# Optimization experiments

Hardware: AMD Instinct MI355X
Metric: run time of the kernel (lower is better)

The kernel has to match this reference:

```python
import math
import jax, jax.numpy as jnp
import numpy as np

N = 4096        # stocks in cross-section
T = 64          # lookback window
D_FEAT = 158
D_MARKET = 64
D_EMB = 32
D_MODEL = 256
T_NHEAD = 4
S_NHEAD = 4
BETA = 1.0
MAX_LEN = 100


def _pe_table(max_len, d_model):
    pos = np.arange(max_len, dtype=np.float32)[:, None]
    div = np.exp(np.arange(0, d_model, 2, dtype=np.float32) * (-math.log(10000.0) / d_model))
    pe = np.zeros((max_len, d_model), dtype=np.float32)
    pe[:, 0::2] = np.sin(pos * div)
    pe[:, 1::2] = np.cos(pos * div)
    return jnp.asarray(pe)


def setup_inputs() -> dict:
    key = jax.random.key(0)
    ks = jax.random.split(key, 24)
    w = lambda k, shape: jax.random.normal(k, shape, jnp.float32) * 0.02
    inp = {
        'industry_ids': jax.random.randint(ks[0], (N,), 0, 256),
        'stock_features': jax.random.normal(ks[1], (N, T, D_FEAT), jnp.float32),
        'market_features': jax.random.normal(ks[2], (N, T, D_MARKET), jnp.float32),
        'gate_W': w(ks[3], (D_MARKET, D_FEAT)), 'gate_b': jnp.zeros((D_FEAT,), jnp.float32),
        'emb_table': w(ks[4], (256, D_EMB)),
        'proj_W': w(ks[5], (D_FEAT, D_MODEL)), 'proj_b': jnp.zeros((D_MODEL,), jnp.float32),
        'pe': _pe_table(MAX_LEN, D_MODEL),
        'ta_qW': w(ks[6], (D_MODEL, D_MODEL)), 'ta_kW': w(ks[7], (D_MODEL, D_MODEL)), 'ta_vW': w(ks[8], (D_MODEL, D_MODEL)),
        'ta_n1_g': jnp.ones((D_MODEL,), jnp.float32), 'ta_n1_b': jnp.zeros((D_MODEL,), jnp.float32),
        'ta_n2_g': jnp.ones((D_MODEL,), jnp.float32), 'ta_n2_b': jnp.zeros((D_MODEL,), jnp.float32),
        'ta_f1W': w(ks[9], (D_MODEL, D_MODEL)), 'ta_f1b': jnp.zeros((D_MODEL,), jnp.float32),
        'ta_f2W': w(ks[10], (D_MODEL, D_MODEL)), 'ta_f2b': jnp.zeros((D_MODEL,), jnp.float32),
        'agg_W': w(ks[11], (D_MODEL, D_MODEL)),
        'sa_qW': w(ks[12], (D_MODEL + D_EMB, D_MODEL)), 'sa_kW': w(ks[13], (D_MODEL + D_EMB, D_MODEL)),
        'sa_vW': w(ks[14], (D_MODEL, D_MODEL)),
        'sa_n1_g': jnp.ones((D_MODEL,), jnp.float32), 'sa_n1_b': jnp.zeros((D_MODEL,), jnp.float32),
        'sa_n2_g': jnp.ones((D_EMB,), jnp.float32), 'sa_n2_b': jnp.zeros((D_EMB,), jnp.float32),
        'sa_n3_g': jnp.ones((D_MODEL,), jnp.float32), 'sa_n3_b': jnp.zeros((D_MODEL,), jnp.float32),
        'sa_f1W': w(ks[15], (D_MODEL, D_MODEL)), 'sa_f1b': jnp.zeros((D_MODEL,), jnp.float32),
        'sa_f2W': w(ks[16], (D_MODEL, D_MODEL)), 'sa_f2b': jnp.zeros((D_MODEL,), jnp.float32),
        'dec_W': w(ks[17], (D_MODEL, 1)), 'dec_b': jnp.zeros((1,), jnp.float32),
    }
    return inp


def _ln(x, g, b, eps=1e-5):
    m = x.mean(-1, keepdims=True)
    v = ((x - m) ** 2).mean(-1, keepdims=True)
    return (x - m) * jax.lax.rsqrt(v + eps) * g + b


def reference(industry_ids, stock_features, market_features, gate_W, gate_b,
              emb_table, proj_W, proj_b, pe,
              ta_qW, ta_kW, ta_vW, ta_n1_g, ta_n1_b, ta_n2_g, ta_n2_b,
              ta_f1W, ta_f1b, ta_f2W, ta_f2b,
              agg_W,
              sa_qW, sa_kW, sa_vW, sa_n1_g, sa_n1_b, sa_n2_g, sa_n2_b,
              sa_n3_g, sa_n3_b, sa_f1W, sa_f1b, sa_f2W, sa_f2b,
              dec_W, dec_b):
    n, t = stock_features.shape[0], stock_features.shape[1]
    # ---- market gating + embedding + projection + positional encoding ----
    emb = emb_table[industry_ids]                                   # [N, d_emb]
    mkt = market_features[:, -1, :]                                 # [N, d_market]
    gate = D_FEAT * jax.nn.softmax((mkt @ gate_W + gate_b) / BETA, axis=-1)
    x = stock_features * gate[:, None, :]                           # [N, T, d_feat]
    x = x @ proj_W + proj_b + pe[:t]                                # [N, T, d_model]
    # ---- TAttention (per-head temporal attention, no temperature scale) ----
    xn = _ln(x, ta_n1_g, ta_n1_b)
    hd = D_MODEL // T_NHEAD
    q = (xn @ ta_qW).reshape(n, t, T_NHEAD, hd)
    k = (xn @ ta_kW).reshape(n, t, T_NHEAD, hd)
    v = (xn @ ta_vW).reshape(n, t, T_NHEAD, hd)
    attn = jax.nn.softmax(jnp.einsum('nthd,nshd->nhts', q, k), axis=-1)
    ao = jnp.einsum('nhts,nshd->nthd', attn, v).reshape(n, t, D_MODEL)
    xt = xn + ao
    ffn = jax.nn.relu(_ln(xt, ta_n2_g, ta_n2_b) @ ta_f1W + ta_f1b) @ ta_f2W + ta_f2b
    x = xt + ffn                                                    # [N, T, d_model]
    # ---- TemporalAttention aggregation ----
    h = x @ agg_W                                                   # [N, T, d_model]
    lam = jax.nn.softmax(jnp.einsum('ntd,nd->nt', h, h[:, -1, :]), axis=1)
    z = jnp.einsum('nt,ntd->nd', lam, x)                            # [N, d_model]
    # ---- SAttention (cross-sectional attention over stocks) ----
    zn = _ln(z, sa_n1_g, sa_n1_b)
    en = _ln(emb, sa_n2_g, sa_n2_b)
    qk_in = jnp.concatenate([zn, en], axis=-1)                      # [N, d_model+d_emb]
    shd = D_MODEL // S_NHEAD
    q2 = (qk_in @ sa_qW).reshape(n, S_NHEAD, shd)
    k2 = (qk_in @ sa_kW).reshape(n, S_NHEAD, shd)
    v2 = (zn @ sa_vW).reshape(n, S_NHEAD, shd)
    scores = jnp.einsum('nhd,mhd->hnm', q2, k2) / math.sqrt(shd)    # [H, N, N]
    a2 = jax.nn.softmax(scores, axis=-1)
    o2 = jnp.einsum('hnm,mhd->nhd', a2, v2).reshape(n, D_MODEL)
    xt2 = zn + o2
    ffn2 = jax.nn.relu(_ln(xt2, sa_n3_g, sa_n3_b) @ sa_f1W + sa_f1b) @ sa_f2W + sa_f2b
    out = xt2 + ffn2
    # ---- decoder ----
    return out @ dec_W + dec_b                                      # [N, 1]
```

## Files before the change

### kernel.cpp

```cpp
#include <hip/hip_runtime.h>
#include <math.h>

typedef unsigned int uint32;
typedef unsigned short ushort;

typedef __bf16 bf16x8 __attribute__((ext_vector_type(8)));
typedef float f32x4 __attribute__((ext_vector_type(4)));

#define DEV static __device__ __forceinline__

DEV float bf2f(ushort u){ return __builtin_bit_cast(float, ((uint32)u) << 16); }
DEV ushort f2bf(float f){
  uint32 i = __builtin_bit_cast(uint32, f);
  uint32 r = i + 0x7fffu + ((i >> 16) & 1u);
  return (ushort)(r >> 16);
}
DEV float wsum(float v){
  #pragma unroll
  for (int off = 32; off > 0; off >>= 1) v += __shfl_xor(v, off);
  return v;
}

__global__ void k_detect(const ushort* pe, const ushort* n1g, int* dt){
  if (threadIdx.x==0 && blockIdx.x==0){
    int isb = (pe[1]==0x3F80u && n1g[0]==0x3F80u) ? 1 : 0;
    *dt = isb ? 1 : 0;
  }
}

struct CvtArgs { const void* src[33]; ushort* dst[33]; int n[33]; };
__global__ __launch_bounds__(256) void k_cvtbatch(CvtArgs a, const int* dtp){
  int z = blockIdx.y;
  int i = blockIdx.x*256 + threadIdx.x;
  if (i >= a.n[z]) return;
  int sdt = *dtp;
  a.dst[z][i] = sdt ? ((const ushort*)a.src[z])[i] : f2bf(((const float*)a.src[z])[i]);
}

struct TrArgs { const ushort* src[12]; ushort* dst[12]; int ldsrc[12]; int R[12]; int C[12]; int lddst[12]; int RP[12]; };
__global__ __launch_bounds__(256) void k_trbatch(TrArgs a){
  int z = blockIdx.z;
  __shared__ ushort tile[32][33];
  int tx = threadIdx.x & 31, ty = threadIdx.x >> 5;
  int rb = blockIdx.x * 32, cb = blockIdx.y * 32;
  const ushort* src = a.src[z];
  int ld_src = a.ldsrc[z], R = a.R[z], C = a.C[z];
  #pragma unroll
  for (int i = 0; i < 4; i++){
    int r = rb + ty + i*8, c = cb + tx;
    ushort v = 0;
    if (r < R && c < C) v = src[(size_t)r*ld_src + c];
    tile[ty + i*8][tx] = v;
  }
  __syncthreads();
  ushort* dst = a.dst[z];
  int ld_dst = a.lddst[z], RP = a.RP[z];
  #pragma unroll
  for (int i = 0; i < 4; i++){
    int c = cb + ty + i*8, r = rb + tx;
    if (c < C && r < RP) dst[(size_t)c*ld_dst + r] = tile[tx][ty + i*8];
  }
}

__global__ __launch_bounds__(256) void k_transpose(const ushort* __restrict__ src, int ld_src,
    int R, int C, ushort* __restrict__ dst, int ld_dst, int RP)
{
  __shared__ ushort tile[32][33];
  int tx = threadIdx.x & 31, ty = threadIdx.x >> 5;
  int rb = blockIdx.x * 32, cb = blockIdx.y * 32;
  #pragma unroll
  for (int i = 0; i < 4; i++){
    int r = rb + ty + i*8, c = cb + tx;
    ushort v = 0;
    if (r < R && c < C) v = src[(size_t)r*ld_src + c];
    tile[ty + i*8][tx] = v;
  }
  __syncthreads();
  #pragma unroll
  for (int i = 0; i < 4; i++){
    int c = cb + ty + i*8, r = rb + tx;
    if (c < C && r < RP) dst[(size_t)c*ld_dst + r] = tile[tx][ty + i*8];
  }
}

__global__ __launch_bounds__(256) void k_gate(const void* __restrict__ mfv,
    const ushort* __restrict__ gW, const ushort* __restrict__ gb, float* __restrict__ gate,
    const int* dtp)
{
  int n = blockIdx.x, tid = threadIdx.x;
  __shared__ int sdt;
  __shared__ float mkt[64];
  __shared__ float red[256];
  if (tid == 0) sdt = *dtp;
  __syncthreads();
  if (tid < 64){
    size_t idx = ((size_t)n*64 + 63)*64 + tid;
    mkt[tid] = sdt ? bf2f(((const ushort*)mfv)[idx]) : ((const float*)mfv)[idx];
  }
  __syncthreads();
  float lg = -1e30f;
  if (tid < 158){
    float a = bf2f(gb[tid]);
    #pragma unroll 8
    for (int d = 0; d < 64; d++) a += mkt[d] * bf2f(gW[d*158 + tid]);
    lg = a;
  }
  red[tid] = lg; __syncthreads();
  for (int s = 128; s > 0; s >>= 1){ if (tid < s) red[tid] = fmaxf(red[tid], red[tid+s]); __syncthreads(); }
  float mx = red[0]; __syncthreads();
  float p = (tid < 158) ? __expf(lg - mx) : 0.f;
  red[tid] = p; __syncthreads();
  for (int s = 128; s > 0; s >>= 1){ if (tid < s) red[tid] += red[tid+s]; __syncthreads(); }
  float inv = 158.f / red[0];
  if (tid < 158) gate[(size_t)n*158 + tid] = p * inv;
}

__global__ __launch_bounds__(256) void k_ag(const void* __restrict__ sfv, size_t rowoff,
    const float* __restrict__ gate_c, ushort* __restrict__ Ag, int total, const int* dtp)
{
  __shared__ int sdt;
  if (threadIdx.x == 0) sdt = *dtp;
  __syncthreads();
  int idx = blockIdx.x*256 + threadIdx.x;
  if (idx >= total) return;
  int row = idx / 160;
  int d = idx - row*160;
  float v = 0.f;
  if (d < 158){
    int n = row >> 6;
    size_t si = (rowoff + (size_t)row)*158 + d;
    float s = sdt ? bf2f(((const ushort*)sfv)[si]) : ((const float*)sfv)[si];
    v = s * gate_c[(size_t)n*158 + d];
  }
  Ag[idx] = f2bf(v);
}

template<int BM, int BN>
__global__ __launch_bounds__(256) void k_gemm(
    const ushort* __restrict__ A, int lda,
    const ushort* __restrict__ WT, int ldw,
    ushort* __restrict__ C, int ldc,
    const ushort* __restrict__ bias,
    const ushort* __restrict__ resid, int ldr,
    const ushort* __restrict__ pe,
    float scale, int relu, int K)
{
  __shared__ ushort As[BM*40];
  __shared__ ushort Bs[BN*40];

  const int tid = threadIdx.x;
  const int wave = tid >> 6, lane = tid & 63;
  const int quad = lane >> 4, l16 = lane & 15;
  constexpr int WC = BN/64;
  const int wr = wave / WC, wc = wave % WC;
  const int m0 = blockIdx.x * BM, n0 = blockIdx.y * BN;

  f32x4 acc[4][4];
  #pragma unroll
  for (int i = 0; i < 4; i++)
    #pragma unroll
    for (int j = 0; j < 4; j++)
      acc[i][j] = f32x4{0.f, 0.f, 0.f, 0.f};

  for (int k0 = 0; k0 < K; k0 += 32){
    __syncthreads();
    #pragma unroll
    for (int i = 0; i < BM/64; i++){
      int ch = tid + i*256;
      int r = ch >> 2, cw = (ch & 3)*8;
      *reinterpret_cast<uint4*>(&As[r*40 + cw]) =
        *reinterpret_cast<const uint4*>(A + (size_t)(m0+r)*lda + k0 + cw);
    }
    #pragma unroll
    for (int i = 0; i < BN/64; i++){
      int ch = tid + i*256;
      int r = ch >> 2, cw = (ch & 3)*8;
      *reinterpret_cast<uint4*>(&Bs[r*40 + cw]) =
        *reinterpret_cast<const uint4*>(WT + (size_t)(n0+r)*ldw + k0 + cw);
    }
    __syncthreads();
    bf16x8 af[4], bfr[4];
    #pragma unroll
    for (int t = 0; t < 4; t++){
      af[t]  = *reinterpret_cast<const bf16x8*>(&As[(wr*64 + t*16 + l16)*40 + quad*8]);
      bfr[t] = *reinterpret_cast<const bf16x8*>(&Bs[(wc*64 + t*16 + l16)*40 + quad*8]);
    }
    #pragma unroll
    for (int mt = 0; mt < 4; mt++)
      #pragma unroll
      for (int nt = 0; nt < 4; nt++)
        acc[mt][nt] = __builtin_amdgcn_mfma_f32_16x16x32_bf16(af[mt], bfr[nt], acc[mt][nt], 0, 0, 0);
  }

  #pragma unroll
  for (int mt = 0; mt < 4; mt++){
    #pragma unroll
    for (int nt = 0; nt < 4; nt++){
      int col = n0 + wc*64 + nt*16 + l16;
      #pragma unroll
      for (int r = 0; r < 4; r++){
        int row = m0 + wr*64 + mt*16 + quad*4 + r;
        float v = acc[mt][nt][r] * scale;
        if (bias)  v += bf2f(bias[col]);
        if (pe)    v += bf2f(pe[(row & 63)*256 + col]);
        if (relu)  v = fmaxf(v, 0.f);
        if (resid) v += bf2f(resid[(size_t)row*ldr + col]);
        C[(size_t)row*ldc + col] = f2bf(v);
      }
    }
  }
}

__global__ __launch_bounds__(256) void k_ln(const ushort* __restrict__ x,
    const ushort* __restrict__ g, const ushort* __restrict__ b, ushort* __restrict__ y)
{
  int row = blockIdx.x*4 + (threadIdx.x >> 6);
  int lane = threadIdx.x & 63;
  ushort4 u = *reinterpret_cast<const ushort4*>(x + (size_t)row*256 + lane*4);
  float v0 = bf2f(u.x), v1 = bf2f(u.y), v2 = bf2f(u.z), v3 = bf2f(u.w);
  float s = wsum(v0+v1+v2+v3);
  float q = wsum(v0*v0+v1*v1+v2*v2+v3*v3);
  float mean = s * (1.f/256.f);
  float var  = fmaxf(q * (1.f/256.f) - mean*mean, 0.f);
  float rs = rsqrtf(var + 1e-5f);
  ushort4 gg = *reinterpret_cast<const ushort4*>(g + lane*4);
  ushort4 bb = *reinterpret_cast<const ushort4*>(b + lane*4);
  ushort4 o;
  o.x = f2bf((v0-mean)*rs*bf2f(gg.x) + bf2f(bb.x));
  o.y = f2bf((v1-mean)*rs*bf2f(gg.y) + bf2f(bb.y));
  o.z = f2bf((v2-mean)*rs*bf2f(gg.z) + bf2f(bb.z));
  o.w = f2bf((v3-mean)*rs*bf2f(gg.w) + bf2f(bb.w));
  *reinterpret_cast<ushort4*>(y + (size_t)row*256 + lane*4) = o;
}

__global__ __launch_bounds__(64) void k_tattn(
    const ushort* __restrict__ q, const ushort* __restrict__ k,
    const ushort* __restrict__ v, ushort* __restrict__ xnxt)
{
  int n = blockIdx.x >> 2, h = blockIdx.x & 3;
  int lane = threadIdx.x;
  int quad = lane >> 4, l16 = lane & 15;
  __shared__ ushort Pl[64*72];
  __shared__ ushort Vt[64*72];
  size_t base = ((size_t)n*64)*256 + (size_t)h*64;

  f32x4 accs[4][4];
  #pragma unroll
  for (int i = 0; i < 4; i++)
    #pragma unroll
    for (int j = 0; j < 4; j++)
      accs[i][j] = f32x4{0.f, 0.f, 0.f, 0.f};

  #pragma unroll
  for (int ks = 0; ks < 64; ks += 32){
    bf16x8 qf[4], kf[4];
    #pragma unroll
    for (int tt = 0; tt < 4; tt++){
      qf[tt] = *reinterpret_cast<const bf16x8*>(q + base + (size_t)(tt*16 + l16)*256 + ks + quad*8);
      kf[tt] = *reinterpret_cast<const bf16x8*>(k + base + (size_t)(tt*16 + l16)*256 + ks + quad*8);
    }
    #pragma unroll
    for (int mt = 0; mt < 4; mt++)
      #pragma unroll
      for (int nt = 0; nt < 4; nt++)
        accs[mt][nt] = __builtin_amdgcn_mfma_f32_16x16x32_bf16(qf[mt], kf[nt], accs[mt][nt], 0, 0, 0);
  }

  for (int s = 0; s < 64; s++)
    Vt[lane*72 + s] = v[base + (size_t)s*256 + lane];

  #pragma unroll
  for (int mt = 0; mt < 4; mt++){
    #pragma unroll
    for (int r = 0; r < 4; r++){
      float a0 = accs[mt][0][r], a1 = accs[mt][1][r], a2 = accs[mt][2][r], a3 = accs[mt][3][r];
      float mx = fmaxf(fmaxf(a0, a1), fmaxf(a2, a3));
      #pragma unroll
      for (int off = 1; off < 16; off <<= 1) mx = fmaxf(mx, __shfl_xor(mx, off));
      float e0 = __expf(a0-mx), e1 = __expf(a1-mx), e2 = __expf(a2-mx), e3 = __expf(a3-mx);
      float sum = e0+e1+e2+e3;
      #pragma unroll
      for (int off = 1; off < 16; off <<= 1) sum += __shfl_xor(sum, off);
      float inv = 1.f/sum;
      int t = mt*16 + quad*4 + r;
      Pl[t*72 +  0 + l16] = f2bf(e0*inv);
      Pl[t*72 + 16 + l16] = f2bf(e1*inv);
      Pl[t*72 + 32 + l16] = f2bf(e2*inv);
      Pl[t*72 + 48 + l16] = f2bf(e3*inv);
    }
  }
  __syncthreads();

  f32x4 acco[4][4];
  #pragma unroll
  for (int i = 0; i < 4; i++)
    #pragma unroll
    for (int j = 0; j < 4; j++)
      acco[i][j] = f32x4{0.f, 0.f, 0.f, 0.f};

  #pragma unroll
  for (int ks = 0; ks < 64; ks += 32){
    bf16x8 pf[4], vf[4];
    #pragma unroll
    for (int tt = 0; tt < 4; tt++){
      pf[tt] = *reinterpret_cast<const bf16x8*>(&Pl[(tt*16 + l16)*72 + ks + quad*8]);
      vf[tt] = *reinterpret_cast<const bf16x8*>(&Vt[(tt*16 + l16)*72 + ks + quad*8]);
    }
    #pragma unroll
    for (int mt = 0; mt < 4; mt++)
      #pragma unroll
      for (int nt = 0; nt < 4; nt++)
        acco[mt][nt] = __builtin_amdgcn_mfma_f32_16x16x32_bf16(pf[mt], vf[nt], acco[mt][nt], 0, 0, 0);
  }

  #pragma unroll
  for (int mt = 0; mt < 4; mt++)
    #pragma unroll
    for (int nt = 0; nt < 4; nt++)
      #pragma unroll
      for (int r = 0; r < 4; r++){
        int t = mt*16 + quad*4 + r, d = nt*16 + l16;
        size_t g = base + (size_t)t*256 + d;
        xnxt[g] = f2bf(bf2f(xnxt[g]) + acco[mt][nt][r]);
      }
}

__global__ __launch_bounds__(256) void k_lamz(const ushort* __restrict__ h,
    const ushort* __restrict__ x2, float* __restrict__ z)
{
  int n = blockIdx.x, tid = threadIdx.x, wave = tid >> 6, lane = tid & 63;
  __shared__ float hl[256];
  __shared__ float dotv[64];
  __shared__ float lamv[64];
  hl[tid] = bf2f(h[((size_t)n*64 + 63)*256 + tid]);
  __syncthreads();
  float h0 = hl[lane*4], h1 = hl[lane*4+1], h2 = hl[lane*4+2], h3 = hl[lane*4+3];
  for (int tt = 0; tt < 16; tt++){
    int t = wave*16 + tt;
    ushort4 u = *reinterpret_cast<const ushort4*>(h + ((size_t)n*64 + t)*256 + lane*4);
    float p = bf2f(u.x)*h0 + bf2f(u.y)*h1 + bf2f(u.z)*h2 + bf2f(u.w)*h3;
    p = wsum(p);
    if (lane == 0) dotv[t] = p;
  }
  __syncthreads();
  if (wave == 0){
    float vv = dotv[lane];
    float mx = vv;
    #pragma unroll
    for (int off = 32; off > 0; off >>= 1) mx = fmaxf(mx, __shfl_xor(mx, off));
    float e = __expf(vv - mx);
    float s = wsum(e);
    lamv[lane] = e / s;
  }
  __syncthreads();
  float acc = 0.f;
  for (int t = 0; t < 64; t++) acc += lamv[t] * bf2f(x2[((size_t)n*64 + t)*256 + tid]);
  z[(size_t)n*256 + tid] = acc;
}

__global__ __launch_bounds__(64) void k_prep(const float* __restrict__ z,
    const int* __restrict__ ids, const ushort* __restrict__ emb,
    const ushort* __restrict__ g1, const ushort* __restrict__ b1,
    const ushort* __restrict__ g2, const ushort* __restrict__ b2,
    ushort* __restrict__ zn, ushort* __restrict__ qkin)
{
  int n = blockIdx.x, lane = threadIdx.x;
  float4 v = *reinterpret_cast<const float4*>(z + (size_t)n*256 + lane*4);
  float s = wsum(v.x+v.y+v.z+v.w);
  float q = wsum(v.x*v.x+v.y*v.y+v.z*v.z+v.w*v.w);
  float mean = s*(1.f/256.f);
  float var = fmaxf(q*(1.f/256.f) - mean*mean, 0.f);
  float rs = rsqrtf(var + 1e-5f);
  ushort4 gg = *reinterpret_cast<const ushort4*>(g1 + lane*4);
  ushort4 bb = *reinterpret_cast<const ushort4*>(b1 + lane*4);
  ushort4 o;
  o.x = f2bf((v.x-mean)*rs*bf2f(gg.x) + bf2f(bb.x));
  o.y = f2bf((v.y-mean)*rs*bf2f(gg.y) + bf2f(bb.y));
  o.z = f2bf((v.z-mean)*rs*bf2f(gg.z) + bf2f(bb.z));
  o.w = f2bf((v.w-mean)*rs*bf2f(gg.w) + bf2f(bb.w));
  *reinterpret_cast<ushort4*>(zn + (size_t)n*256 + lane*4) = o;
  *reinterpret_cast<ushort4*>(qkin + (size_t)n*288 + lane*4) = o;
  int id = ids[n];
  float ev = (lane < 32) ? bf2f(emb[(size_t)id*32 + lane]) : 0.f;
  float se = ev, sq = ev*ev;
  #pragma unroll
  for (int off = 1; off < 32; off <<= 1){ se += __shfl_xor(se, off); sq += __shfl_xor(sq, off); }
  if (lane < 32){
    float m2 = se*(1.f/32.f);
    float va = fmaxf(sq*(1.f/32.f) - m2*m2, 0.f);
    float r2 = rsqrtf(va + 1e-5f);
    qkin[(size_t)n*288 + 256 + lane] = f2bf((ev-m2)*r2*bf2f(g2[lane]) + bf2f(b2[lane]));
  }
}

__global__ __launch_bounds__(256) void k_xattn(
    const ushort* __restrict__ qk, const ushort* __restrict__ vT,
    const ushort* __restrict__ zn, ushort* __restrict__ xt2)
{
  int rb = blockIdx.x, h = blockIdx.y;
  int tid = threadIdx.x, wave = tid >> 6, lane = tid & 63;
  int quad = lane >> 4, l16 = lane & 15;
  int q0 = rb*64 + wave*16;

  bf16x8 qf[2];
  #pragma unroll
  for (int s = 0; s < 2; s++)
    qf[s] = *reinterpret_cast<const bf16x8*>(qk + (size_t)(q0 + l16)*512 + h*64 + s*32 + quad*8);

  float m[4]  = {-1e30f,-1e30f,-1e30f,-1e30f};
  float l[4]  = {0.f,0.f,0.f,0.f};
  f32x4 acc[4];
  #pragma unroll
  for (int nd = 0; nd < 4; nd++) acc[nd] = f32x4{0.f,0.f,0.f,0.f};

  __shared__ ushort Pl[4][16*72];

  for (int kt = 0; kt < 64; kt++){
    int kb = kt*64;
    f32x4 s4[4];
    #pragma unroll
    for (int nt = 0; nt < 4; nt++){
      f32x4 a = f32x4{0.f,0.f,0.f,0.f};
      #pragma unroll
      for (int s = 0; s < 2; s++){
        bf16x8 kf = *reinterpret_cast<const bf16x8*>(
            qk + (size_t)(kb + nt*16 + l16)*512 + 256 + h*64 + s*32 + quad*8);
        a = __builtin_amdgcn_mfma_f32_16x16x32_bf16(qf[s], kf, a, 0, 0, 0);
      }
      s4[nt] = a;
    }
    float alpha[4];
    #pragma unroll
    for (int r = 0; r < 4; r++){
      float v0 = s4[0][r]*0.125f, v1 = s4[1][r]*0.125f, v2 = s4[2][r]*0.125f, v3 = s4[3][r]*0.125f;
      float mx = fmaxf(fmaxf(v0,v1), fmaxf(v2,v3));
      #pragma unroll
      for (int off = 1; off < 16; off <<= 1) mx = fmaxf(mx, __shfl_xor(mx, off));
      float mnew = fmaxf(m[r], mx);
      alpha[r] = __expf(m[r] - mnew);
      float e0 = __expf(v0-mnew), e1 = __expf(v1-mnew), e2 = __expf(v2-mnew), e3 = __expf(v3-mnew);
      float ps = e0+e1+e2+e3;
      #pragma unroll
      for (int off = 1; off < 16; off <<= 1) ps += __shfl_xor(ps, off);
      l[r] = l[r]*alpha[r] + ps;
      m[r] = mnew;
      int t = quad*4 + r;
      Pl[wave][t*72 +  0 + l16] = f2bf(e0);
      Pl[wave][t*72 + 16 + l16] = f2bf(e1);
      Pl[wave][t*72 + 32 + l16] = f2bf(e2);
      Pl[wave][t*72 + 48 + l16] = f2bf(e3);
    }
    #pragma unroll
    for (int nd = 0; nd < 4; nd++)
      #pragma unroll
      for (int r = 0; r < 4; r++)
        acc[nd][r] *= alpha[r];
    __syncthreads();
    #pragma unroll
    for (int s = 0; s < 2; s++){
      bf16x8 pf = *reinterpret_cast<const bf16x8*>(&Pl[wave][l16*72 + s*32 + quad*8]);
      #pragma unroll
      for (int nd = 0; nd < 4; nd++){
        bf16x8 vf = *reinterpret_cast<const bf16x8*>(
            vT + (size_t)(h*64 + nd*16 + l16)*4096 + kb + s*32 + quad*8);
        acc[nd] = __builtin_amdgcn_mfma_f32_16x16x32_bf16(pf, vf, acc[nd], 0, 0, 0);
      }
    }
    __syncthreads();
  }

  #pragma unroll
  for (int nd = 0; nd < 4; nd++)
    #pragma unroll
    for (int r = 0; r < 4; r++){
      int row = q0 + quad*4 + r;
      int col = h*64 + nd*16 + l16;
      float val = acc[nd][r] / l[r] + bf2f(zn[(size_t)row*256 + col]);
      xt2[(size_t)row*256 + col] = f2bf(val);
    }
}

__global__ __launch_bounds__(64) void k_decode(const ushort* __restrict__ xv,
    const ushort* __restrict__ dW, const ushort* __restrict__ db, void* out, const int* dtp)
{
  int n = blockIdx.x, lane = threadIdx.x;
  ushort4 u = *reinterpret_cast<const ushort4*>(xv + (size_t)n*256 + lane*4);
  ushort4 w = *reinterpret_cast<const ushort4*>(dW + lane*4);
  float acc = bf2f(u.x)*bf2f(w.x) + bf2f(u.y)*bf2f(w.y) + bf2f(u.z)*bf2f(w.z) + bf2f(u.w)*bf2f(w.w);
  acc = wsum(acc);
  if (lane == 0){
    float r = acc + bf2f(db[0]);
    if (*dtp) ((ushort*)out)[n] = f2bf(r);
    else      ((float*)out)[n]  = r;
  }
}

extern "C" void kernel_launch(void* const* d_in, const int* in_sizes, int n_in,
                              void* d_out, int out_size, void* d_ws, size_t ws_size,
                              hipStream_t stream)
{
  (void)in_sizes; (void)n_in; (void)out_size;
  const int*  ids = (const int*)d_in[0];
  const void* sf  = d_in[1];
  const void* mf  = d_in[2];

  auto padsz = [](size_t b)->size_t{ return (b + 255) & ~(size_t)255; };
  size_t fixedB = padsz((size_t)4096*158*4) + padsz((size_t)4096*256*4)
                + 6*padsz((size_t)4096*256*2)
                + padsz((size_t)4096*512*2)
                + padsz((size_t)256*4096*2)
                + padsz((size_t)4096*288*2)
                + (size_t)4*1024*1024;
  auto tierB = [&](int NCp)->size_t{
    size_t MCp = (size_t)NCp*64;
    return fixedB + 4*padsz(MCp*256*2) + padsz(MCp*160*2);
  };
  int NC = 64;
  if      (tierB(4096) <= ws_size) NC = 4096;
  else if (tierB(1024) <= ws_size) NC = 1024;
  else if (tierB(256)  <= ws_size) NC = 256;
  const int NCHUNK = 4096 / NC;
  const int MC = NC * 64;

  char* ws = (char*)d_ws;
  size_t off = 0;
  auto alloc = [&](size_t bytes)->char*{ char* p = ws + off; off += (bytes + 255) & ~(size_t)255; return p; };
  int* dt = (int*)alloc(256);
  ushort* C0 = (ushort*)alloc((size_t)MC*256*2);
  ushort* C1 = (ushort*)alloc((size_t)MC*256*2);
  ushort* C2 = (ushort*)alloc((size_t)MC*256*2);
  ushort* C3 = (ushort*)alloc((size_t)MC*256*2);
  ushort* Ag = (ushort*)alloc((size_t)MC*160*2);
  float*  gate = (float*)alloc((size_t)4096*158*4);
  float*  z    = (float*)alloc((size_t)4096*256*4);
  ushort* zn   = (ushort*)alloc((size_t)4096*256*2);
  ushort* q2k2 = (ushort*)alloc((size_t)4096*512*2);
  ushort* v2   = (ushort*)alloc((size_t)4096*256*2);
  ushort* vT   = (ushort*)alloc((size_t)256*4096*2);
  ushort* xt2  = (ushort*)alloc((size_t)4096*256*2);
  ushort* n3   = (ushort*)alloc((size_t)4096*256*2);
  ushort* h2   = (ushort*)alloc((size_t)4096*256*2);
  ushort* xv   = (ushort*)alloc((size_t)4096*256*2);
  ushort* qkin = (ushort*)alloc((size_t)4096*288*2);

  auto cvalloc = [&](int n)->ushort*{ return (ushort*)alloc((size_t)n*2); };
  ushort* gWc   = cvalloc(64*158);
  ushort* gbc   = cvalloc(158);
  ushort* embc  = cvalloc(256*32);
  ushort* projWc= cvalloc(158*256);
  ushort* projbc= cvalloc(256);
  ushort* pec   = cvalloc(100*256);
  ushort* taqWc = cvalloc(65536);
  ushort* takWc = cvalloc(65536);
  ushort* tavWc = cvalloc(65536);
  ushort* n1gc  = cvalloc(256);
  ushort* n1bc  = cvalloc(256);
  ushort* n2gc  = cvalloc(256);
  ushort* n2bc  = cvalloc(256);
  ushort* f1Wc  = cvalloc(65536);
  ushort* f1bc  = cvalloc(256);
  ushort* f2Wc  = cvalloc(65536);
  ushort* f2bc  = cvalloc(256);
  ushort* aggWc = cvalloc(65536);
  ushort* saqWc = cvalloc(288*256);
  ushort* sakWc = cvalloc(288*256);
  ushort* savWc = cvalloc(65536);
  ushort* sn1gc = cvalloc(256);
  ushort* sn1bc = cvalloc(256);
  ushort* sn2gc = cvalloc(32);
  ushort* sn2bc = cvalloc(32);
  ushort* sn3gc = cvalloc(256);
  ushort* sn3bc = cvalloc(256);
  ushort* sf1Wc = cvalloc(65536);
  ushort* sf1bc = cvalloc(256);
  ushort* sf2Wc = cvalloc(65536);
  ushort* sf2bc = cvalloc(256);
  ushort* decWc = cvalloc(256);
  ushort* decbc = cvalloc(1);
  ushort* projWT = cvalloc(256*160);
  ushort* taqWT  = cvalloc(65536);
  ushort* takWT  = cvalloc(65536);
  ushort* tavWT  = cvalloc(65536);
  ushort* f1WT   = cvalloc(65536);
  ushort* f2WT   = cvalloc(65536);
  ushort* aggWT  = cvalloc(65536);
  ushort* savWT  = cvalloc(65536);
  ushort* sf1WT  = cvalloc(65536);
  ushort* sf2WT  = cvalloc(65536);
  ushort* qk2WT  = cvalloc(512*288);

  dim3 b256(256), b64(64);

  k_detect<<<1, 64, 0, stream>>>((const ushort*)d_in[8], (const ushort*)d_in[12], dt);

  CvtArgs ca;
  int ci = 0;
  auto addcv = [&](int idx, ushort* dst, int n){ ca.src[ci]=d_in[idx]; ca.dst[ci]=dst; ca.n[ci]=n; ci++; };
  addcv(3,  gWc,   64*158);  addcv(4,  gbc,   158);     addcv(5,  embc,  256*32);
  addcv(6,  projWc,158*256); addcv(7,  projbc,256);     addcv(8,  pec,   100*256);
  addcv(9,  taqWc, 65536);   addcv(10, takWc, 65536);   addcv(11, tavWc, 65536);
  addcv(12, n1gc,  256);     addcv(13, n1bc,  256);     addcv(14, n2gc,  256);
  addcv(15, n2bc,  256);     addcv(16, f1Wc,  65536);   addcv(17, f1bc,  256);
  addcv(18, f2Wc,  65536);   addcv(19, f2bc,  256);     addcv(20, aggWc, 65536);
  addcv(21, saqWc, 288*256); addcv(22, sakWc, 288*256); addcv(23, savWc, 65536);
  addcv(24, sn1gc, 256);     addcv(25, sn1bc, 256);     addcv(26, sn2gc, 32);
  addcv(27, sn2bc, 32);      addcv(28, sn3gc, 256);     addcv(29, sn3bc, 256);
  addcv(30, sf1Wc, 65536);   addcv(31, sf1bc, 256);     addcv(32, sf2Wc, 65536);
  addcv(33, sf2bc, 256);     addcv(34, decWc, 256);     addcv(35, decbc, 1);
  k_cvtbatch<<<dim3(288, 33), b256, 0, stream>>>(ca, dt);

  TrArgs ta;
  int ti = 0;
  auto addtr = [&](const ushort* src, int ldsrc, int R, int C, ushort* dst, int lddst, int RP){
    ta.src[ti]=src; ta.ldsrc[ti]=ldsrc; ta.R[ti]=R; ta.C[ti]=C; ta.dst[ti]=dst; ta.lddst[ti]=lddst; ta.RP[ti]=RP; ti++;
  };
  addtr(projWc, 256, 158, 256, projWT, 160, 160);
  addtr(taqWc,  256, 256, 256, taqWT,  256, 256);
  addtr(takWc,  256, 256, 256, takWT,  256, 256);
  addtr(tavWc,  256, 256, 256, tavWT,  256, 256);
  addtr(f1Wc,   256, 256, 256, f1WT,   256, 256);
  addtr(f2Wc,   256, 256, 256, f2WT,   256, 256);
  addtr(aggWc,  256, 256, 256, aggWT,  256, 256);
  addtr(saqWc,  256, 288, 256, qk2WT,            288, 288);
  addtr(sakWc,  256, 288, 256, qk2WT + 256*288,  288, 288);
  addtr(savWc,  256, 256, 256, savWT,  256, 256);
  addtr(sf1Wc,  256, 256, 256, sf1WT,  256, 256);
  addtr(sf2Wc,  256, 256, 256, sf2WT,  256, 256);
  k_trbatch<<<dim3(9, 8, 12), b256, 0, stream>>>(ta);

  k_gate<<<4096, b256, 0, stream>>>(mf, gWc, gbc, gate, dt);

  for (int c = 0; c < NCHUNK; c++){
    const float* gate_c = gate + (size_t)c*NC*158;
    float*       z_c    = z    + (size_t)c*NC*256;
    size_t rowoff = (size_t)c*MC;

    k_ag<<<(MC*160)/256, b256, 0, stream>>>(sf, rowoff, gate_c, Ag, MC*160, dt);
    k_gemm<128,128><<<dim3(MC/128, 2), b256, 0, stream>>>(Ag,160, projWT,160, C0,256,
        projbc, nullptr,0, pec, 1.f, 0, 160);
    k_ln<<<MC/4, b256, 0, stream>>>(C0, n1gc, n1bc, C1);
    k_gemm<128,128><<<dim3(MC/128, 2), b256, 0, stream>>>(C1,256, taqWT,256, C0,256,
        nullptr, nullptr,0, nullptr, 1.f, 0, 256);
    k_gemm<128,128><<<dim3(MC/128, 2), b256, 0, stream>>>(C1,256, takWT,256, C2,256,
        nullptr, nullptr,0, nullptr, 1.f, 0, 256);
    k_gemm<128,128><<<dim3(MC/128, 2), b256, 0, stream>>>(C1,256, tavWT,256, C3,256,
        nullptr, nullptr,0, nullptr, 1.f, 0, 256);
    k_tattn<<<NC*4, b64, 0, stream>>>(C0, C2, C3, C1);
    k_ln<<<MC/4, b256, 0, stream>>>(C1, n2gc, n2bc, C0);
    k_gemm<128,128><<<dim3(MC/128, 2), b256, 0, stream>>>(C0,256, f1WT,256, C2,256,
        f1bc, nullptr,0, nullptr, 1.f, 1, 256);
    k_gemm<128,128><<<dim3(MC/128, 2), b256, 0, stream>>>(C2,256, f2WT,256, C3,256,
        f2bc, C1,256, nullptr, 1.f, 0, 256);
    k_gemm<128,128><<<dim3(MC/128, 2), b256, 0, stream>>>(C3,256, aggWT,256, C0,256,
        nullptr, nullptr,0, nullptr, 1.f, 0, 256);
    k_lamz<<<NC, b256, 0, stream>>>(C0, C3, z_c);
  }

  k_prep<<<4096, b64, 0, stream>>>(z, ids, embc, sn1gc, sn1bc, sn2gc, sn2bc, zn, qkin);
  k_gemm<128,128><<<dim3(32,4,1), b256, 0, stream>>>(qkin,288, qk2WT,288, q2k2,512,
      nullptr, nullptr,0, nullptr, 1.f, 0, 288);
  k_gemm<128,128><<<dim3(32,2,1), b256, 0, stream>>>(zn,256, savWT,256, v2,256,
      nullptr, nullptr,0, nullptr, 1.f, 0, 256);
  k_transpose<<<dim3(128, 8), b256, 0, stream>>>(v2, 256, 4096, 256, vT, 4096, 4096);
  k_xattn<<<dim3(64, 4), b256, 0, stream>>>(q2k2, vT, zn, xt2);

  k_ln<<<1024, b256, 0, stream>>>(xt2, sn3gc, sn3bc, n3);
  k_gemm<128,128><<<dim3(32,2,1), b256, 0, stream>>>(n3,256, sf1WT,256, h2,256,
      sf1bc, nullptr,0, nullptr, 1.f, 1, 256);
  k_gemm<128,128><<<dim3(32,2,1), b256, 0, stream>>>(h2,256, sf2WT,256, xv,256,
      sf2bc, xt2,256, nullptr, 1.f, 0, 256);
  k_decode<<<4096, b64, 0, stream>>>(xv, decWc, decbc, d_out, dt);
}
```

Measured before the change: 1.895 ms.

## Fuse temporal Q/K/V projections into one GEMM and prefetch GEMM tiles in registers

Concatenates the transposed temporal-attention Q, K and V weights into one 768-column matrix. The three projections now run as a single GEMM writing an interleaved QKV buffer, and the attention kernel reads q, k and v from that buffer at different column offsets. The GEMM main loop also loads the next K-slice of A and B into registers while the current slice is being computed, a simple software-pipelining step meant to hide global load latency. The cost is a larger workspace for the QKV buffer, which may lower the chunk tier that fits, plus extra register pressure in the GEMM.

```diff
diff --git a/kernel.cpp b/kernel.cpp
--- a/kernel.cpp
+++ b/kernel.cpp
@@ -155,6 +155,23 @@
   const int wr = wave / WC, wc = wave % WC;
   const int m0 = blockIdx.x * BM, n0 = blockIdx.y * BN;
 
+  constexpr int NA = BM/64, NB = BN/64;
+  int chA[NA], cwA[NA], chB[NB], cwB[NB];
+  const ushort* aptr[NA];
+  const ushort* bptr[NB];
+  #pragma unroll
+  for (int i = 0; i < NA; i++){
+    int ch = tid + i*256;
+    chA[i] = ch >> 2; cwA[i] = (ch & 3)*8;
+    aptr[i] = A + (size_t)(m0 + chA[i])*lda + cwA[i];
+  }
+  #pragma unroll
+  for (int i = 0; i < NB; i++){
+    int ch = tid + i*256;
+    chB[i] = ch >> 2; cwB[i] = (ch & 3)*8;
+    bptr[i] = WT + (size_t)(n0 + chB[i])*ldw + cwB[i];
+  }
+
   f32x4 acc[4][4];
   #pragma unroll
   for (int i = 0; i < 4; i++)
@@ -162,23 +179,29 @@
     for (int j = 0; j < 4; j++)
       acc[i][j] = f32x4{0.f, 0.f, 0.f, 0.f};
 
+  uint4 ra[NA], rb[NB];
+  #pragma unroll
+  for (int i = 0; i < NA; i++) ra[i] = *reinterpret_cast<const uint4*>(aptr[i]);
+  #pragma unroll
+  for (int i = 0; i < NB; i++) rb[i] = *reinterpret_cast<const uint4*>(bptr[i]);
+
   for (int k0 = 0; k0 < K; k0 += 32){
     __syncthreads();
     #pragma unroll
-    for (int i = 0; i < BM/64; i++){
-      int ch = tid + i*256;
-      int r = ch >> 2, cw = (ch & 3)*8;
-      *reinterpret_cast<uint4*>(&As[r*40 + cw]) =
-        *reinterpret_cast<const uint4*>(A + (size_t)(m0+r)*lda + k0 + cw);
-    }
-    #pragma unroll
-    for (int i = 0; i < BN/64; i++){
-      int ch = tid + i*256;
-      int r = ch >> 2, cw = (ch & 3)*8;
-      *reinterpret_cast<uint4*>(&Bs[r*40 + cw]) =
-        *reinterpret_cast<const uint4*>(WT + (size_t)(n0+r)*ldw + k0 + cw);
-    }
+    for (int i = 0; i < NA; i++)
+      *reinterpret_cast<uint4*>(&As[chA[i]*40 + cwA[i]]) = ra[i];
+    #pragma unroll
+    for (int i = 0; i < NB; i++)
+      *reinterpret_cast<uint4*>(&Bs[chB[i]*40 + cwB[i]]) = rb[i];
     __syncthreads();
+
+    if (k0 + 32 < K){
+      #pragma unroll
+      for (int i = 0; i < NA; i++) ra[i] = *reinterpret_cast<const uint4*>(aptr[i] + k0 + 32);
+      #pragma unroll
+      for (int i = 0; i < NB; i++) rb[i] = *reinterpret_cast<const uint4*>(bptr[i] + k0 + 32);
+    }
+
     bf16x8 af[4], bfr[4];
     #pragma unroll
     for (int t = 0; t < 4; t++){
@@ -234,15 +257,15 @@
 }
 
 __global__ __launch_bounds__(64) void k_tattn(
-    const ushort* __restrict__ q, const ushort* __restrict__ k,
-    const ushort* __restrict__ v, ushort* __restrict__ xnxt)
+    const ushort* __restrict__ qkv, ushort* __restrict__ xnxt)
 {
   int n = blockIdx.x >> 2, h = blockIdx.x & 3;
   int lane = threadIdx.x;
   int quad = lane >> 4, l16 = lane & 15;
   __shared__ ushort Pl[64*72];
   __shared__ ushort Vt[64*72];
-  size_t base = ((size_t)n*64)*256 + (size_t)h*64;
+  size_t rowb = (size_t)n*64;
+  const int co_q = h*64, co_k = 256 + h*64, co_v = 512 + h*64;
 
   f32x4 accs[4][4];
   #pragma unroll
@@ -256,8 +279,8 @@
     bf16x8 qf[4], kf[4];
     #pragma unroll
     for (int tt = 0; tt < 4; tt++){
-      qf[tt] = *reinterpret_cast<const bf16x8*>(q + base + (size_t)(tt*16 + l16)*256 + ks + quad*8);
-      kf[tt] = *reinterpret_cast<const bf16x8*>(k + base + (size_t)(tt*16 + l16)*256 + ks + quad*8);
+      qf[tt] = *reinterpret_cast<const bf16x8*>(qkv + (rowb + tt*16 + l16)*768 + co_q + ks + quad*8);
+      kf[tt] = *reinterpret_cast<const bf16x8*>(qkv + (rowb + tt*16 + l16)*768 + co_k + ks + quad*8);
     }
     #pragma unroll
     for (int mt = 0; mt < 4; mt++)
@@ -267,7 +290,7 @@
   }
 
   for (int s = 0; s < 64; s++)
-    Vt[lane*72 + s] = v[base + (size_t)s*256 + lane];
+    Vt[lane*72 + s] = qkv[(rowb + s)*768 + co_v + lane];
 
   #pragma unroll
   for (int mt = 0; mt < 4; mt++){
@@ -320,7 +343,7 @@
       #pragma unroll
       for (int r = 0; r < 4; r++){
         int t = mt*16 + quad*4 + r, d = nt*16 + l16;
-        size_t g = base + (size_t)t*256 + d;
+        size_t g = (rowb + t)*256 + h*64 + d;
         xnxt[g] = f2bf(bf2f(xnxt[g]) + acco[mt][nt][r]);
       }
 }
@@ -513,7 +536,7 @@
                 + (size_t)4*1024*1024;
   auto tierB = [&](int NCp)->size_t{
     size_t MCp = (size_t)NCp*64;
-    return fixedB + 4*padsz(MCp*256*2) + padsz(MCp*160*2);
+    return fixedB + 4*padsz(MCp*256*2) + padsz(MCp*160*2) + padsz(MCp*768*2);
   };
   int NC = 64;
   if      (tierB(4096) <= ws_size) NC = 4096;
@@ -531,6 +554,7 @@
   ushort* C2 = (ushort*)alloc((size_t)MC*256*2);
   ushort* C3 = (ushort*)alloc((size_t)MC*256*2);
   ushort* Ag = (ushort*)alloc((size_t)MC*160*2);
+  ushort* QKV = (ushort*)alloc((size_t)MC*768*2);
   float*  gate = (float*)alloc((size_t)4096*158*4);
   float*  z    = (float*)alloc((size_t)4096*256*4);
   ushort* zn   = (ushort*)alloc((size_t)4096*256*2);
@@ -578,9 +602,7 @@
   ushort* decWc = cvalloc(256);
   ushort* decbc = cvalloc(1);
   ushort* projWT = cvalloc(256*160);
-  ushort* taqWT  = cvalloc(65536);
-  ushort* takWT  = cvalloc(65536);
-  ushort* tavWT  = cvalloc(65536);
+  ushort* qkvWT  = cvalloc(768*256);
   ushort* f1WT   = cvalloc(65536);
   ushort* f2WT   = cvalloc(65536);
   ushort* aggWT  = cvalloc(65536);
@@ -615,9 +637,9 @@
     ta.src[ti]=src; ta.ldsrc[ti]=ldsrc; ta.R[ti]=R; ta.C[ti]=C; ta.dst[ti]=dst; ta.lddst[ti]=lddst; ta.RP[ti]=RP; ti++;
   };
   addtr(projWc, 256, 158, 256, projWT, 160, 160);
-  addtr(taqWc,  256, 256, 256, taqWT,  256, 256);
-  addtr(takWc,  256, 256, 256, takWT,  256, 256);
-  addtr(tavWc,  256, 256, 256, tavWT,  256, 256);
+  addtr(taqWc,  256, 256, 256, qkvWT,            256, 256);
+  addtr(takWc,  256, 256, 256, qkvWT + 256*256,  256, 256);
+  addtr(tavWc,  256, 256, 256, qkvWT + 512*256,  256, 256);
   addtr(f1Wc,   256, 256, 256, f1WT,   256, 256);
   addtr(f2Wc,   256, 256, 256, f2WT,   256, 256);
   addtr(aggWc,  256, 256, 256, aggWT,  256, 256);
@@ -639,13 +661,9 @@
     k_gemm<128,128><<<dim3(MC/128, 2), b256, 0, stream>>>(Ag,160, projWT,160, C0,256,
         projbc, nullptr,0, pec, 1.f, 0, 160);
     k_ln<<<MC/4, b256, 0, stream>>>(C0, n1gc, n1bc, C1);
-    k_gemm<128,128><<<dim3(MC/128, 2), b256, 0, stream>>>(C1,256, taqWT,256, C0,256,
+    k_gemm<128,128><<<dim3(MC/128, 6), b256, 0, stream>>>(C1,256, qkvWT,256, QKV,768,
         nullptr, nullptr,0, nullptr, 1.f, 0, 256);
-    k_gemm<128,128><<<dim3(MC/128, 2), b256, 0, stream>>>(C1,256, takWT,256, C2,256,
-        nullptr, nullptr,0, nullptr, 1.f, 0, 256);
-    k_gemm<128,128><<<dim3(MC/128, 2), b256, 0, stream>>>(C1,256, tavWT,256, C3,256,
-        nullptr, nullptr,0, nullptr, 1.f, 0, 256);
-    k_tattn<<<NC*4, b64, 0, stream>>>(C0, C2, C3, C1);
+    k_tattn<<<NC*4, b64, 0, stream>>>(QKV, C1);
     k_ln<<<MC/4, b256, 0, stream>>>(C1, n2gc, n2bc, C0);
     k_gemm<128,128><<<dim3(MC/128, 2), b256, 0, stream>>>(C0,256, f1WT,256, C2,256,
         f1bc, nullptr,0, nullptr, 1.f, 1, 256);
```

Result: slower. 2.653 ms (+39.9%).
